# Kernel optimization log

Measured on AMD Instinct MI355X. Metric: run time of the kernel, lower is better.

Reference implementation:

```python
import jax, jax.numpy as jnp
import numpy as np
import math

E = 768      # embed_dim
N = 16       # ssm state_dim
K = 4        # d_conv
R = 48       # dt_rank = ceil(E/16)
DEPTH = 4
V = 32000    # vocab
B = 2
L = 1024
T = 100
H = 4 * E    # mlp hidden


def layer_norm(x, g, b):
    mu = jnp.mean(x, axis=-1, keepdims=True)
    var = jnp.mean(jnp.square(x - mu), axis=-1, keepdims=True)
    return (x - mu) * jax.lax.rsqrt(var + 1e-5) * g + b


def sin_emb(t, dim):
    half = dim // 2
    freqs = jnp.exp(-math.log(10000.0) * jnp.arange(half, dtype=jnp.float32) / half)
    args = t.astype(jnp.float32)[:, None] * freqs
    return jnp.concatenate([jnp.sin(args), jnp.cos(args)], axis=-1)


def ssm_forward(x, z_w, p_w, conv_w, dtp_w, dtp_b, A_log, Dp, out_w):
    # x: (B, L, E)
    z = x @ z_w.T
    params = x @ p_w.T                      # (B, L, R+2N)
    dt_un, _B_unused, Cp = jnp.split(params, [R, R + N], axis=-1)
    dt = jax.nn.softplus(dt_un @ dtp_w.T + dtp_b)   # (B, L, E)
    # depthwise causal conv (torch pads both sides d_conv-1 then trims -> left pad only)
    xc = jax.lax.conv_general_dilated(
        jnp.transpose(x, (0, 2, 1)), conv_w, (1,), [(K - 1, 0)],
        feature_group_count=E, dimension_numbers=('NCH', 'OIH', 'NCH'))
    u = jax.nn.silu(jnp.transpose(xc, (0, 2, 1)))   # (B, L, E)
    A = -jnp.exp(A_log)                              # (E, N)
    A_t = jnp.exp(dt[..., None] * A)                 # (B, L, E, N)
    B_t = jnp.where(jnp.abs(A) < 1e-5, dt[..., None], (A_t - 1.0) / (A + 1e-10))
    # recurrence exactly as source: h[0]=B[0]*u[0]; h[t]=A[t-1]*h[t-1]+B[t-1]*u[t-1]
    h0 = B_t[:, 0] * u[:, 0, :, None]                # (B, E, N)
    xs = (jnp.moveaxis(A_t[:, :-1], 1, 0),
          jnp.moveaxis(B_t[:, :-1], 1, 0),
          jnp.moveaxis(u[:, :-1], 1, 0))
    def step(h, inp):
        a, b, uu = inp
        h = a * h + b * uu[..., None]
        return h, h
    _, hs = jax.lax.scan(step, h0, xs)               # (L-1, B, E, N)
    h_all = jnp.concatenate([h0[None], hs], axis=0)  # (L, B, E, N)
    y = jnp.einsum('bln,lben->ble', Cp, h_all)
    y = y + u * Dp
    return (y * jax.nn.silu(z)) @ out_w.T


def setup_inputs() -> dict:
    key = jax.random.key(0)
    ks = list(jax.random.split(key, 32))
    it = iter(ks)
    def nrm(shape, fan_in):
        return jax.random.normal(next(it), shape, jnp.float32) * np.sqrt(2.0 / fan_in)
    d = {}
    d['tokens'] = jax.random.randint(next(it), (B, L), 0, V + 1)
    d['timesteps'] = jax.random.randint(next(it), (B,), 0, T)
    d['tok_emb'] = jax.random.normal(next(it), (V + 1, E), jnp.float32) * 0.02
    d['time_w1'] = nrm((H, E), E); d['time_b1'] = jnp.zeros((H,), jnp.float32)
    d['time_w2'] = nrm((E, H), H); d['time_b2'] = jnp.zeros((E,), jnp.float32)
    d['ln1_g'] = jnp.ones((DEPTH, E), jnp.float32); d['ln1_b'] = jnp.zeros((DEPTH, E), jnp.float32)
    d['z_w'] = nrm((DEPTH, E, E), E)
    d['p_w'] = nrm((DEPTH, R + 2 * N, E), E)
    d['conv_w'] = jax.random.normal(next(it), (DEPTH, E, 1, K), jnp.float32) * np.sqrt(1.0 / K)
    s = R ** -0.5 * 0.1
    d['dtp_w'] = jax.random.uniform(next(it), (DEPTH, E, R), jnp.float32, -s, s)
    d['dtp_b'] = jnp.full((DEPTH, E), math.log(math.expm1(0.001)), jnp.float32)
    d['A_log'] = jnp.tile(jnp.log(jnp.arange(1, N + 1, dtype=jnp.float32)), (DEPTH, E, 1))
    d['D_param'] = jnp.ones((DEPTH, E), jnp.float32)
    d['out_w'] = nrm((DEPTH, E, E), E)
    d['ln2_g'] = jnp.ones((DEPTH, E), jnp.float32); d['ln2_b'] = jnp.zeros((DEPTH, E), jnp.float32)
    d['mlp_w1'] = nrm((DEPTH, H, E), E); d['mlp_b1'] = jnp.zeros((DEPTH, H), jnp.float32)
    d['mlp_w2'] = nrm((DEPTH, E, H), H); d['mlp_b2'] = jnp.zeros((DEPTH, E), jnp.float32)
    d['lnout_g'] = jnp.ones((E,), jnp.float32); d['lnout_b'] = jnp.zeros((E,), jnp.float32)
    d['head_w'] = nrm((V, E), E); d['head_b'] = jnp.zeros((V,), jnp.float32)
    return d


def reference(tokens, timesteps, tok_emb, time_w1, time_b1, time_w2, time_b2,
              ln1_g, ln1_b, z_w, p_w, conv_w, dtp_w, dtp_b, A_log, D_param, out_w,
              ln2_g, ln2_b, mlp_w1, mlp_b1, mlp_w2, mlp_b2,
              lnout_g, lnout_b, head_w, head_b):
    temb = sin_emb(timesteps, E)
    temb = jax.nn.silu(temb @ time_w1.T + time_b1) @ time_w2.T + time_b2
    x = tok_emb[tokens] + temb[:, None, :]           # (B, L, E)
    for i in range(DEPTH):
        x = x + ssm_forward(layer_norm(x, ln1_g[i], ln1_b[i]),
                            z_w[i], p_w[i], conv_w[i], dtp_w[i], dtp_b[i],
                            A_log[i], D_param[i], out_w[i])
        h = layer_norm(x, ln2_g[i], ln2_b[i])
        h = jax.nn.gelu(h @ mlp_w1[i].T + mlp_b1[i], approximate=False) @ mlp_w2[i].T + mlp_b2[i]
        x = x + h
    x = layer_norm(x, lnout_g, lnout_b)
    return x @ head_w.T + head_b                     # (B, L, V)
```

## Files before the change

### kernel.cpp

```cpp
#include <hip/hip_runtime.h>
#include <math.h>

#define EE 768
#define NS 16
#define RR 48
#define NDEPTH 4
#define NB 2
#define NL 1024
#define NH 3072
#define NV 32000
#define M_ROWS (NB*NL)
#define NC 64
#define CL 16
#define ZPW 896
#define LOG2E 1.44269504088896f
#define LN2   0.69314718055995f

typedef __attribute__((ext_vector_type(8))) __bf16 bf16x8;
typedef __attribute__((ext_vector_type(4))) __bf16 bf16x4;
typedef __attribute__((ext_vector_type(4))) float f32x4;

__device__ __forceinline__ void gl_lds16(const __bf16* g, __bf16* l){
  __builtin_amdgcn_global_load_lds(
      (const __attribute__((address_space(1))) void*)g,
      (__attribute__((address_space(3))) void*)l, 16, 0, 0);
}

enum { BE_STORE=0, BE_BIAS=1, BE_RESID=2, BE_BIAS_RESID=3, BE_BIAS_GELU_B16=4,
       BE_STORE_ZP=5 };

template<int EPI, int BMT, int BNT>
__global__ __launch_bounds__(256) void gemm_bf16(const __bf16* __restrict__ A,
    const __bf16* __restrict__ W, const float* __restrict__ bias,
    void* __restrict__ Cv, float* __restrict__ dtf, float* __restrict__ aux,
    int N, int K, int gx, int gy)
{
  const int nwg = gx*gy;
  const int orig = blockIdx.x;
  const int q = nwg >> 3, r = nwg & 7;
  const int xcd = orig & 7, bse = orig >> 3;
  int wg = (xcd < r ? xcd*(q+1) : r*(q+1) + (xcd-r)*q) + bse;
  const int GN = 16;
  const int per = gy*GN;
  const int g = wg / per;
  const int gstart = g*GN;
  const int gw0 = gx - gstart;
  const int gw = (GN < gw0) ? GN : gw0;
  const int local = wg - g*per;
  const int bx = gstart + local % gw;
  const int by = local / gw;

  constexpr int MFR = BMT/32;
  constexpr int NFR = BNT/32;
  __shared__ __bf16 As[BMT][64];
  __shared__ __bf16 Ws[BNT][64];
  const int bm = by*BMT, bn = bx*BNT;
  const int tid = threadIdx.x;
  const int w = tid>>6, lane = tid&63;
  const int wr = w>>1, wc = w&1;
  const int fr = lane&15, kg = lane>>4;
  const int sr8 = lane>>3;
  const int sg  = lane&7;
  const int ksrc = ((sg ^ sr8) & 7)*8;

  f32x4 acc[MFR][NFR];
  #pragma unroll
  for (int m=0;m<MFR;m++)
    #pragma unroll
    for (int n=0;n<NFR;n++)
      acc[m][n] = (f32x4){0.f,0.f,0.f,0.f};

  for (int k0=0;k0<K;k0+=64){
    const __bf16* gA = A + (size_t)(bm + w*(BMT/4) + sr8)*K + k0 + ksrc;
    #pragma unroll
    for (int c8=0;c8<BMT/32;c8++)
      gl_lds16(gA + (size_t)(c8*8)*K, &As[w*(BMT/4) + c8*8][0]);
    const __bf16* gW = W + (size_t)(bn + w*(BNT/4) + sr8)*K + k0 + ksrc;
    #pragma unroll
    for (int c8=0;c8<BNT/32;c8++)
      gl_lds16(gW + (size_t)(c8*8)*K, &Ws[w*(BNT/4) + c8*8][0]);
    __syncthreads();
    #pragma unroll
    for (int kk=0;kk<2;kk++){
      const int sp = (((kg + kk*4) ^ (fr&7)) & 7) * 8;
      bf16x8 af[MFR], bfr[NFR];
      #pragma unroll
      for (int m=0;m<MFR;m++) af[m]  = *(const bf16x8*)&As[wr*(BMT/2) + m*16 + fr][sp];
      #pragma unroll
      for (int n=0;n<NFR;n++) bfr[n] = *(const bf16x8*)&Ws[wc*(BNT/2) + n*16 + fr][sp];
      #pragma unroll
      for (int m=0;m<MFR;m++)
        #pragma unroll
        for (int n=0;n<NFR;n++)
          acc[m][n] = __builtin_amdgcn_mfma_f32_16x16x32_bf16(af[m], bfr[n], acc[m][n], 0,0,0);
    }
    __syncthreads();
  }

  float* Cf = (float*)Cv;
  __bf16* Cb = (__bf16*)Cv;
  #pragma unroll
  for (int m=0;m<MFR;m++){
    int row = bm + wr*(BMT/2) + m*16 + kg*4;
    #pragma unroll
    for (int n=0;n<NFR;n++){
      int col = bn + wc*(BNT/2) + n*16 + fr;
      float bsv = 0.f;
      if (EPI==BE_BIAS || EPI==BE_BIAS_RESID || EPI==BE_BIAS_GELU_B16)
        bsv = bias[col];
      #pragma unroll
      for (int rr2=0;rr2<4;rr2++){
        float v = acc[m][n][rr2];
        size_t idx = (size_t)(row+rr2)*N + col;
        if (EPI==BE_STORE)            Cf[idx] = v;
        else if (EPI==BE_BIAS)        Cf[idx] = v + bsv;
        else if (EPI==BE_RESID)       Cf[idx] += v;
        else if (EPI==BE_BIAS_RESID)  Cf[idx] += v + bsv;
        else if (EPI==BE_BIAS_GELU_B16){
          float xg = v + bsv; Cb[idx] = (__bf16)(0.5f*xg*(1.f+erff(xg*0.70710678118654752f)));
        } else if (EPI==BE_STORE_ZP){
          if (col < 768)                    Cb[(size_t)(row+rr2)*EE + col] = (__bf16)v;
          else if (col < 816)               dtf[(size_t)(row+rr2)*RR + (col-768)] = v;
          else if (col >= 832 && col < 848) aux[(size_t)(row+rr2)*16 + (col-832)] = v;
        }
      }
    }
  }
}

__global__ __launch_bounds__(512) void gemm_head3p(const __bf16* __restrict__ A,
    const __bf16* __restrict__ W, const float* __restrict__ bias,
    float* __restrict__ C)
{
  const int gx = NV/128, gy = M_ROWS/256;
  const int nwg = gx*gy;
  const int orig = blockIdx.x;
  const int q = nwg >> 3;
  const int xcd = orig & 7, bse = orig >> 3;
  int wg = xcd*q + bse;
  const int GN = 32;
  const int per = gy*GN;
  const int g = wg / per;
  const int gstart = g*GN;
  const int gw0 = gx - gstart;
  const int gw = (GN < gw0) ? GN : gw0;
  const int local = wg - g*per;
  const int bx = gstart + local % gw;
  const int by = local / gw;

  __shared__ __bf16 Ah[3][256][64];
  __shared__ __bf16 Wh[3][128][64];
  const int bm = by*256, bn = bx*128;
  const int tid = threadIdx.x;
  const int w = tid>>6, lane = tid&63;
  const int wr = w>>1, wc = w&1;
  const int fr = lane&15, kg = lane>>4;
  const int ksrc = (((lane&7) ^ ((lane>>3)&7)) & 7)*8;

  f32x4 acc[4][4];
  #pragma unroll
  for (int m=0;m<4;m++)
    #pragma unroll
    for (int n=0;n<4;n++)
      acc[m][n] = (f32x4){0.f,0.f,0.f,0.f};

  auto stage = [&](int bufp, int kt){
    const __bf16* gA = A + (size_t)(bm + w*8 + (lane>>3))*EE + kt*64 + ksrc;
    #pragma unroll
    for (int j=0;j<4;j++)
      gl_lds16(gA + (size_t)(j*64)*EE, &Ah[bufp][j*64 + w*8][0]);
    const __bf16* gW = W + (size_t)(bn + w*8 + (lane>>3))*EE + kt*64 + ksrc;
    #pragma unroll
    for (int j=0;j<2;j++)
      gl_lds16(gW + (size_t)(j*64)*EE, &Wh[bufp][j*64 + w*8][0]);
  };

  stage(0, 0);
  stage(1, 1);
  #pragma unroll
  for (int t=0;t<12;t++){
    if (t < 11) asm volatile("s_waitcnt vmcnt(6)\n\ts_barrier" ::: "memory");
    else        asm volatile("s_waitcnt vmcnt(0)\n\ts_barrier" ::: "memory");
    const int b_ = t % 3;
    #pragma unroll
    for (int kk=0;kk<2;kk++){
      const int sp = (((kg + kk*4) ^ (fr&7)) & 7) * 8;
      bf16x8 af[4], bfr[4];
      #pragma unroll
      for (int m=0;m<4;m++) af[m]  = *(const bf16x8*)&Ah[b_][wr*64 + m*16 + fr][sp];
      #pragma unroll
      for (int n=0;n<4;n++) bfr[n] = *(const bf16x8*)&Wh[b_][wc*64 + n*16 + fr][sp];
      #pragma unroll
      for (int m=0;m<4;m++)
        #pragma unroll
        for (int n=0;n<4;n++)
          acc[m][n] = __builtin_amdgcn_mfma_f32_16x16x32_bf16(af[m], bfr[n], acc[m][n], 0,0,0);
    }
    if (t+2 < 12) stage((t+2)%3, t+2);
  }

  #pragma unroll
  for (int m=0;m<4;m++){
    int row = bm + wr*64 + m*16 + kg*4;
    #pragma unroll
    for (int n=0;n<4;n++){
      int col = bn + wc*64 + n*16 + fr;
      float bsv = bias[col];
      #pragma unroll
      for (int rr2=0;rr2<4;rr2++)
        C[(size_t)(row+rr2)*NV + col] = acc[m][n][rr2] + bsv;
    }
  }
}

#define S1E 2752512LL
#define S2E 5111808LL
#define S3E 14548992LL
#define S4E 23986176LL
#define STOT 48562176LL

__global__ void f2b_all(const float* __restrict__ zw, const float* __restrict__ pw,
                        const float* __restrict__ ow, const float* __restrict__ m1,
                        const float* __restrict__ m2, const float* __restrict__ hw,
                        __bf16* __restrict__ o){
  long long idx = ((long long)blockIdx.x*256 + threadIdx.x)*4;
  if (idx >= STOT) return;
  float4 v;
  if (idx < S1E){
    long long layer = idx / (ZPW*EE);
    int rem = (int)(idx - layer*(ZPW*EE));
    int row = rem / EE, col = rem - (rem/EE)*EE;
    if (row < 768)      v = *(const float4*)(zw + ((size_t)layer*EE + row)*EE + col);
    else if (row < 848) v = *(const float4*)(pw + ((size_t)layer*80 + (row-768))*EE + col);
    else                v = make_float4(0.f,0.f,0.f,0.f);
  }
  else if (idx < S2E) v = *(const float4*)(ow + (idx - S1E));
  else if (idx < S3E) v = *(const float4*)(m1 + (idx - S2E));
  else if (idx < S4E) v = *(const float4*)(m2 + (idx - S3E));
  else                v = *(const float4*)(hw + (idx - S4E));
  bf16x4 rb = { (__bf16)v.x, (__bf16)v.y, (__bf16)v.z, (__bf16)v.w };
  *(bf16x4*)(o+idx) = rb;
}

__global__ __launch_bounds__(256) void ln_kernel(const float* __restrict__ x,
    const float* __restrict__ gp, const float* __restrict__ bp, __bf16* __restrict__ yb)
{
  int row = blockIdx.x*4 + (threadIdx.x>>6);
  int lane = threadIdx.x & 63;
  const float* xr = x + (size_t)row*EE;
  float4 v0 = *(const float4*)(xr + lane*4);
  float4 v1 = *(const float4*)(xr + 256 + lane*4);
  float4 v2 = *(const float4*)(xr + 512 + lane*4);
  float s = (v0.x+v0.y)+(v0.z+v0.w) + (v1.x+v1.y)+(v1.z+v1.w) + (v2.x+v2.y)+(v2.z+v2.w);
  float q = v0.x*v0.x+v0.y*v0.y+v0.z*v0.z+v0.w*v0.w
          + v1.x*v1.x+v1.y*v1.y+v1.z*v1.z+v1.w*v1.w
          + v2.x*v2.x+v2.y*v2.y+v2.z*v2.z+v2.w*v2.w;
  #pragma unroll
  for (int m=1;m<64;m<<=1){ s += __shfl_xor(s, m, 64); q += __shfl_xor(q, m, 64); }
  float mu  = s*(1.f/768.f);
  float var = q*(1.f/768.f) - mu*mu;
  float inv = 1.0f/sqrtf(var + 1e-5f);
  __bf16* ybr = yb + (size_t)row*EE;
  #pragma unroll
  for (int p=0;p<3;p++){
    const float4 v = (p==0)? v0 : (p==1)? v1 : v2;
    int o = p*256 + lane*4;
    float4 gg = *(const float4*)(gp + o);
    float4 bb = *(const float4*)(bp + o);
    bf16x4 ov = { (__bf16)((v.x-mu)*inv*gg.x + bb.x),
                  (__bf16)((v.y-mu)*inv*gg.y + bb.y),
                  (__bf16)((v.z-mu)*inv*gg.z + bb.z),
                  (__bf16)((v.w-mu)*inv*gg.w + bb.w) };
    *(bf16x4*)(ybr + o) = ov;
  }
}

__global__ void sinemb_kernel(const int* __restrict__ timesteps, float* __restrict__ emb){
  int i = blockIdx.x*256+threadIdx.x;
  if (i >= NB*EE) return;
  int b = i/EE, e = i - b*EE;
  int half = EE/2;
  int j = (e<half)? e : e-half;
  float freq = expf(-logf(10000.f)*(float)j/(float)half);
  float arg = (float)timesteps[b]*freq;
  emb[i] = (e<half)? sinf(arg) : cosf(arg);
}

__global__ void time_mlp1(const float* __restrict__ emb, const float* __restrict__ w1,
                          const float* __restrict__ b1, float* __restrict__ thid){
  int wid = (blockIdx.x*256 + threadIdx.x)>>6;
  int lane = threadIdx.x & 63;
  int b = wid / NH, h = wid - b*NH;
  const float* er = emb + b*EE;
  const float* wr = w1 + (size_t)h*EE;
  float s = 0.f;
  #pragma unroll
  for (int j=0;j<EE/64;j++) s = fmaf(er[j*64+lane], wr[j*64+lane], s);
  #pragma unroll
  for (int m=1;m<64;m<<=1) s += __shfl_xor(s, m, 64);
  if (lane==0){
    s += b1[h];
    thid[wid] = s/(1.f+expf(-s));
  }
}

__global__ void time_mlp2(const float* __restrict__ thid, const float* __restrict__ w2,
                          const float* __restrict__ b2, float* __restrict__ temb){
  int wid = (blockIdx.x*256 + threadIdx.x)>>6;
  int lane = threadIdx.x & 63;
  int b = wid / EE, e = wid - b*EE;
  const float* tr = thid + b*NH;
  const float* wr = w2 + (size_t)e*NH;
  float s = 0.f;
  #pragma unroll
  for (int j=0;j<NH/64;j++) s = fmaf(tr[j*64+lane], wr[j*64+lane], s);
  #pragma unroll
  for (int m=1;m<64;m<<=1) s += __shfl_xor(s, m, 64);
  if (lane==0) temb[wid] = s + b2[e];
}

__global__ void embed_kernel(const int* __restrict__ tokens, const float* __restrict__ tok_emb,
                             const float* __restrict__ temb, float* __restrict__ x){
  int idx = blockIdx.x*256+threadIdx.x;
  int e = idx % EE; int bl = idx / EE; int b = bl / NL;
  int tok = tokens[bl];
  x[idx] = tok_emb[(size_t)tok*EE + e] + temb[b*EE + e];
}

__device__ __forceinline__ float dot48(const float* __restrict__ row, const float* wdf){
  float a0=0.f,a1=0.f,a2=0.f,a3=0.f;
  #pragma unroll
  for (int j=0;j<12;j++){
    float4 v = *(const float4*)(row + j*4);
    a0 = fmaf(v.x, wdf[j*4+0], a0);
    a1 = fmaf(v.y, wdf[j*4+1], a1);
    a2 = fmaf(v.z, wdf[j*4+2], a2);
    a3 = fmaf(v.w, wdf[j*4+3], a3);
  }
  return (a0+a1)+(a2+a3);
}
__device__ __forceinline__ float softplus_f(float x){
  return fmaxf(x,0.f) + LN2*log2f(1.f + exp2f(-LOG2E*fabsf(x)));
}
__device__ __forceinline__ float silu_f(float x){
  return x/(1.f + exp2f(-LOG2E*x));
}

__global__ __launch_bounds__(256) void scan_fused(
    const __bf16* __restrict__ xnb, const float* __restrict__ dtun,
    const float* __restrict__ dtw, const float* __restrict__ dtbias,
    const float* __restrict__ cwp, const float* __restrict__ A_log,
    const float* __restrict__ Dp, const float* __restrict__ cpf,
    const __bf16* __restrict__ zgb, __bf16* __restrict__ gb)
{
  __shared__ float Pl[NC][4][NS];
  __shared__ float Sl[NC][4][NS];
  __shared__ float dtc_l[CL][256];
  __shared__ float uc_l[CL+1][256];
  const int tid = threadIdx.x;
  const int e_l = tid & 3, c = tid >> 2;
  const int b  = blockIdx.x / (EE/4);
  const int eg = blockIdx.x % (EE/4);
  const int e  = eg*4 + e_l;

  float wdf[48];
  #pragma unroll
  for (int j=0;j<12;j++){
    float4 v = *(const float4*)(dtw + (size_t)e*RR + j*4);
    wdf[j*4]=v.x; wdf[j*4+1]=v.y; wdf[j*4+2]=v.z; wdf[j*4+3]=v.w;
  }
  float4 cw = *(const float4*)(cwp + e*4);
  float bias = dtbias[e];
  float Dv = Dp[e];
  float Av2[NS], iAv[NS];
  #pragma unroll
  for (int n4=0;n4<4;n4++){
    float4 v = *(const float4*)(A_log + (size_t)e*NS + n4*4);
    float a0=-exp2f(LOG2E*v.x), a1=-exp2f(LOG2E*v.y), a2=-exp2f(LOG2E*v.z), a3=-exp2f(LOG2E*v.w);
    Av2[n4*4+0]=a0*LOG2E; Av2[n4*4+1]=a1*LOG2E; Av2[n4*4+2]=a2*LOG2E; Av2[n4*4+3]=a3*LOG2E;
    iAv[n4*4+0]=1.f/(a0+1e-10f); iAv[n4*4+1]=1.f/(a1+1e-10f);
    iAv[n4*4+2]=1.f/(a2+1e-10f); iAv[n4*4+3]=1.f/(a3+1e-10f);
  }
  const __bf16* xcol = xnb + (size_t)b*NL*EE + e;
  const float* dtrow0 = dtun + (size_t)b*NL*RR;
  const int cs = c*CL;

  {
    float xw0,xw1,xw2,xw3;
    int prow = (c==0)? 0 : cs-1;
    xw0 = (prow-3>=0)? (float)xcol[(size_t)(prow-3)*EE] : 0.f;
    xw1 = (prow-2>=0)? (float)xcol[(size_t)(prow-2)*EE] : 0.f;
    xw2 = (prow-1>=0)? (float)xcol[(size_t)(prow-1)*EE] : 0.f;
    xw3 = (float)xcol[(size_t)prow*EE];
    float up  = silu_f(cw.x*xw0 + cw.y*xw1 + cw.z*xw2 + cw.w*xw3);
    float dtp_ = softplus_f(dot48(dtrow0 + (size_t)prow*RR, wdf) + bias);
    float h[NS];
    float sumdt = 0.f;
    #pragma unroll
    for (int n=0;n<NS;n++) h[n]=0.f;
    for (int i=0;i<CL;i++){
      int tt = cs+i;
      bool z0 = (tt==0);
      dtc_l[i][tid] = dtp_;
      uc_l[i][tid]  = up;
      sumdt += dtp_;
      #pragma unroll
      for (int n=0;n<NS;n++){
        float at = exp2f(dtp_*Av2[n]);
        float bt = (at-1.f)*iAv[n];
        float s = bt*up;
        h[n] = z0 ? s : fmaf(at, h[n], s);
      }
      if (tt>0){
        xw0=xw1; xw1=xw2; xw2=xw3; xw3 = (float)xcol[(size_t)tt*EE];
        up  = silu_f(cw.x*xw0 + cw.y*xw1 + cw.z*xw2 + cw.w*xw3);
        dtp_ = softplus_f(dot48(dtrow0 + (size_t)tt*RR, wdf) + bias);
      }
    }
    uc_l[CL][tid] = up;
    #pragma unroll
    for (int n4=0;n4<4;n4++){
      float4 pv;
      if (c==0) pv = make_float4(0.f,0.f,0.f,0.f);
      else pv = make_float4(exp2f(Av2[n4*4+0]*sumdt), exp2f(Av2[n4*4+1]*sumdt),
                            exp2f(Av2[n4*4+2]*sumdt), exp2f(Av2[n4*4+3]*sumdt));
      *(float4*)&Pl[c][e_l][n4*4] = pv;
      *(float4*)&Sl[c][e_l][n4*4] = make_float4(h[n4*4],h[n4*4+1],h[n4*4+2],h[n4*4+3]);
    }
  }
  __syncthreads();
  if (tid < 64){
    int el2 = tid & 3, n = tid >> 2;
    float hh = 0.f;
    for (int cc=0; cc<NC; cc++){
      float pp = Pl[cc][el2][n], ss = Sl[cc][el2][n];
      Pl[cc][el2][n] = hh;
      hh = fmaf(pp, hh, ss);
    }
  }
  __syncthreads();
  {
    float h[NS];
    #pragma unroll
    for (int n4=0;n4<4;n4++){
      float4 v = *(const float4*)&Pl[c][e_l][n4*4];
      h[n4*4]=v.x; h[n4*4+1]=v.y; h[n4*4+2]=v.z; h[n4*4+3]=v.w;
    }
    #pragma unroll
    for (int i=0;i<CL;i++){
      int tt = cs+i;
      bool z0 = (tt==0);
      float dtp_ = dtc_l[i][tid];
      float up   = uc_l[i][tid];
      float ucur = uc_l[i+1][tid];
      #pragma unroll
      for (int n=0;n<NS;n++){
        float at = exp2f(dtp_*Av2[n]);
        float bt = (at-1.f)*iAv[n];
        float s = bt*up;
        h[n] = z0 ? s : fmaf(at, h[n], s);
      }
      const float* cpr = cpf + (size_t)(b*NL+tt)*16;
      float y = 0.f;
      #pragma unroll
      for (int n4=0;n4<4;n4++){
        float4 cv = *(const float4*)(cpr + n4*4);
        y = fmaf(cv.x, h[n4*4], y);   y = fmaf(cv.y, h[n4*4+1], y);
        y = fmaf(cv.z, h[n4*4+2], y); y = fmaf(cv.w, h[n4*4+3], y);
      }
      float zv = (float)zgb[(size_t)(b*NL+tt)*EE + e];
      gb[(size_t)(b*NL+tt)*EE + e] = (__bf16)((y + ucur*Dv)*silu_f(zv));
    }
  }
}

extern "C" void kernel_launch(void* const* d_in, const int* in_sizes, int n_in,
                              void* d_out, int out_size, void* d_ws, size_t ws_size,
                              hipStream_t stream) {
  const int*   tokens    = (const int*)d_in[0];
  const int*   timesteps = (const int*)d_in[1];
  const float* tok_emb   = (const float*)d_in[2];
  const float* time_w1   = (const float*)d_in[3];
  const float* time_b1   = (const float*)d_in[4];
  const float* time_w2   = (const float*)d_in[5];
  const float* time_b2   = (const float*)d_in[6];
  const float* ln1_g     = (const float*)d_in[7];
  const float* ln1_b     = (const float*)d_in[8];
  const float* z_w       = (const float*)d_in[9];
  const float* p_w       = (const float*)d_in[10];
  const float* conv_w    = (const float*)d_in[11];
  const float* dtp_w     = (const float*)d_in[12];
  const float* dtp_b     = (const float*)d_in[13];
  const float* A_log     = (const float*)d_in[14];
  const float* D_param   = (const float*)d_in[15];
  const float* out_w     = (const float*)d_in[16];
  const float* ln2_g     = (const float*)d_in[17];
  const float* ln2_b     = (const float*)d_in[18];
  const float* mlp_w1    = (const float*)d_in[19];
  const float* mlp_b1    = (const float*)d_in[20];
  const float* mlp_w2    = (const float*)d_in[21];
  const float* mlp_b2    = (const float*)d_in[22];
  const float* lnout_g   = (const float*)d_in[23];
  const float* lnout_b   = (const float*)d_in[24];
  const float* head_w    = (const float*)d_in[25];
  const float* head_b    = (const float*)d_in[26];
  float* out = (float*)d_out;

  float* ws = (float*)d_ws;
  float* x      = ws;
  float* cpf    = x    + (size_t)M_ROWS*EE;
  float* dtun   = cpf  + (size_t)M_ROWS*16;
  float* emb    = dtun + (size_t)M_ROWS*RR;
  float* thid   = emb + NB*EE;
  __bf16* xnb   = (__bf16*)(thid + NB*NH);
  __bf16* zgb   = xnb + (size_t)M_ROWS*EE;
  __bf16* gb    = zgb + (size_t)M_ROWS*EE;
  __bf16* hidb  = gb  + (size_t)M_ROWS*EE;
  __bf16* wzp   = hidb + (size_t)M_ROWS*NH;
  __bf16* wout  = wzp  + (size_t)NDEPTH*ZPW*EE;
  __bf16* wm1   = wout + (size_t)NDEPTH*EE*EE;
  __bf16* wm2   = wm1  + (size_t)NDEPTH*NH*EE;
  __bf16* whead = wm2  + (size_t)NDEPTH*EE*NH;

  f2b_all<<<(int)(STOT/4/256), 256, 0, stream>>>(z_w, p_w, out_w, mlp_w1, mlp_w2, head_w, wzp);

  sinemb_kernel<<<(NB*EE+255)/256, 256, 0, stream>>>(timesteps, emb);
  time_mlp1<<<NB*NH/4, 256, 0, stream>>>(emb, time_w1, time_b1, thid);
  time_mlp2<<<NB*EE/4, 256, 0, stream>>>(thid, time_w2, time_b2, emb);
  embed_kernel<<<M_ROWS*EE/256, 256, 0, stream>>>(tokens, tok_emb, emb, x);

  const int scan_grid = NB*EE/4;

  for (int i=0;i<NDEPTH;i++){
    const float* dtw = dtp_w + (size_t)i*EE*RR;
    const float* dtb = dtp_b + i*EE;
    const float* cwp = conv_w + (size_t)i*EE*4;
    const float* al  = A_log + (size_t)i*EE*NS;
    ln_kernel<<<M_ROWS/4, 256, 0, stream>>>(x, ln1_g + i*EE, ln1_b + i*EE, xnb);
    gemm_bf16<BE_STORE_ZP,64,64><<<14*32, 256, 0, stream>>>(
        xnb, wzp + (size_t)i*ZPW*EE, nullptr, zgb, dtun, cpf, ZPW, EE, 14, 32);
    scan_fused<<<scan_grid, 256, 0, stream>>>(xnb, dtun, dtw, dtb, cwp, al,
        D_param + i*EE, cpf, zgb, gb);
    gemm_bf16<BE_RESID,64,64><<<12*32, 256, 0, stream>>>(
        gb, wout + (size_t)i*EE*EE, nullptr, x, nullptr, nullptr, EE, EE, 12, 32);
    ln_kernel<<<M_ROWS/4, 256, 0, stream>>>(x, ln2_g + i*EE, ln2_b + i*EE, xnb);
    gemm_bf16<BE_BIAS_GELU_B16,64,128><<<24*32, 256, 0, stream>>>(
        xnb, wm1 + (size_t)i*NH*EE, mlp_b1 + i*NH, hidb, nullptr, nullptr, NH, EE, 24, 32);
    gemm_bf16<BE_BIAS_RESID,64,64><<<12*32, 256, 0, stream>>>(
        hidb, wm2 + (size_t)i*EE*NH, mlp_b2 + i*EE, x, nullptr, nullptr, EE, NH, 12, 32);
  }
  ln_kernel<<<M_ROWS/4, 256, 0, stream>>>(x, lnout_g, lnout_b, xnb);
  gemm_head3p<<<(NV/128)*(M_ROWS/256), 512, 0, stream>>>(xnb, whead, head_b, out);
}
```

Measured before the change: 775.4 us.

## Triple-buffer GEMM LDS tiles with async global-to-LDS prefetch two tiles ahead

Converts the bf16 MFMA GEMM main loop from single-buffered load/sync/compute to a three-stage LDS ring. Tiles are prefetched two k-steps ahead with global_load_lds, and explicit vmcnt waits plus a single barrier per iteration replace the two __syncthreads. This is meant to hide global memory latency behind MFMA work. It triples shared memory use, which may lower occupancy, and it relies on hand-coded vmcnt counts that must match the per-thread load count.

```diff
diff --git a/kernel.cpp b/kernel.cpp
--- a/kernel.cpp
+++ b/kernel.cpp
@@ -52,8 +52,9 @@
 
   constexpr int MFR = BMT/32;
   constexpr int NFR = BNT/32;
-  __shared__ __bf16 As[BMT][64];
-  __shared__ __bf16 Ws[BNT][64];
+  constexpr int LPT = BMT/32 + BNT/32;
+  __shared__ __bf16 As[3][BMT][64];
+  __shared__ __bf16 Ws[3][BNT][64];
   const int bm = by*BMT, bn = bx*BNT;
   const int tid = threadIdx.x;
   const int w = tid>>6, lane = tid&63;
@@ -70,31 +71,43 @@
     for (int n=0;n<NFR;n++)
       acc[m][n] = (f32x4){0.f,0.f,0.f,0.f};
 
-  for (int k0=0;k0<K;k0+=64){
-    const __bf16* gA = A + (size_t)(bm + w*(BMT/4) + sr8)*K + k0 + ksrc;
+  auto stage = [&](int buf, int kt){
+    const __bf16* gA = A + (size_t)(bm + w*(BMT/4) + sr8)*K + kt*64 + ksrc;
     #pragma unroll
     for (int c8=0;c8<BMT/32;c8++)
-      gl_lds16(gA + (size_t)(c8*8)*K, &As[w*(BMT/4) + c8*8][0]);
-    const __bf16* gW = W + (size_t)(bn + w*(BNT/4) + sr8)*K + k0 + ksrc;
+      gl_lds16(gA + (size_t)(c8*8)*K, &As[buf][w*(BMT/4) + c8*8][0]);
+    const __bf16* gW = W + (size_t)(bn + w*(BNT/4) + sr8)*K + kt*64 + ksrc;
     #pragma unroll
     for (int c8=0;c8<BNT/32;c8++)
-      gl_lds16(gW + (size_t)(c8*8)*K, &Ws[w*(BNT/4) + c8*8][0]);
-    __syncthreads();
+      gl_lds16(gW + (size_t)(c8*8)*K, &Ws[buf][w*(BNT/4) + c8*8][0]);
+  };
+
+  const int ntiles = K >> 6;
+  stage(0, 0);
+  if (ntiles > 1) stage(1, 1);
+  for (int t=0; t<ntiles; t++){
+    if (t+1 < ntiles){
+      if constexpr (LPT==4) asm volatile("s_waitcnt vmcnt(4)\n\ts_barrier" ::: "memory");
+      else                  asm volatile("s_waitcnt vmcnt(6)\n\ts_barrier" ::: "memory");
+    } else {
+      asm volatile("s_waitcnt vmcnt(0)\n\ts_barrier" ::: "memory");
+    }
+    const int b_ = t % 3;
     #pragma unroll
     for (int kk=0;kk<2;kk++){
       const int sp = (((kg + kk*4) ^ (fr&7)) & 7) * 8;
       bf16x8 af[MFR], bfr[NFR];
       #pragma unroll
-      for (int m=0;m<MFR;m++) af[m]  = *(const bf16x8*)&As[wr*(BMT/2) + m*16 + fr][sp];
-      #pragma unroll
-      for (int n=0;n<NFR;n++) bfr[n] = *(const bf16x8*)&Ws[wc*(BNT/2) + n*16 + fr][sp];
+      for (int m=0;m<MFR;m++) af[m]  = *(const bf16x8*)&As[b_][wr*(BMT/2) + m*16 + fr][sp];
+      #pragma unroll
+      for (int n=0;n<NFR;n++) bfr[n] = *(const bf16x8*)&Ws[b_][wc*(BNT/2) + n*16 + fr][sp];
       #pragma unroll
       for (int m=0;m<MFR;m++)
         #pragma unroll
         for (int n=0;n<NFR;n++)
           acc[m][n] = __builtin_amdgcn_mfma_f32_16x16x32_bf16(af[m], bfr[n], acc[m][n], 0,0,0);
     }
-    __syncthreads();
+    if (t+2 < ntiles) stage((t+2)%3, t+2);
   }
 
   float* Cf = (float*)Cv;
```

After: 774.3 us, median of 2. About the same (-0.1%).
